# Performance work log

Hardware: AMD Instinct MI355X
Metric: run time of the kernel (lower is better)

## Reference

```python
import jax, jax.numpy as jnp
import numpy as np

NUM_HEADS = 8
HEAD_SIZE = 64  # hidden_dim // num_heads = 512 // 8
SCALE = 1.0 / np.sqrt(HEAD_SIZE).astype(np.float32)
CAUSAL = True


def setup_inputs() -> dict:
    key = jax.random.key(0)
    k1, k2, k3 = jax.random.split(key, 3)
    b, s, d = 4, 2048, 512
    x = jax.random.normal(k1, (b, s, d), dtype=jnp.float32)
    w_qkv = jax.random.normal(k2, (d, 3 * d), dtype=jnp.float32) * 0.02
    b_qkv = jnp.zeros((3 * d,), dtype=jnp.float32)
    w_out = jax.random.normal(k3, (d, d), dtype=jnp.float32) * 0.02
    b_out = jnp.zeros((d,), dtype=jnp.float32)
    return {"x": x, "w_qkv": w_qkv, "b_qkv": b_qkv, "w_out": w_out, "b_out": b_out}


def reference(x, w_qkv, b_qkv, w_out, b_out):
    b, s, d = x.shape
    h, hd = NUM_HEADS, HEAD_SIZE
    qkv = x @ w_qkv + b_qkv                      # (b, s, 3d)
    q, k, v = jnp.split(qkv, 3, axis=-1)
    # (b, s, d) -> (b, h, s, hd)
    q = q.reshape(b, s, h, hd).transpose(0, 2, 1, 3)
    k = k.reshape(b, s, h, hd).transpose(0, 2, 1, 3)
    v = v.reshape(b, s, h, hd).transpose(0, 2, 1, 3)
    scores = jnp.einsum('bhqd,bhkd->bhqk', q, k) * SCALE  # (b, h, s, s)
    if CAUSAL:
        causal_mask = jnp.triu(jnp.ones((s, s), dtype=bool), k=1)
        scores = jnp.where(causal_mask, -jnp.inf, scores)
    attn = jax.nn.softmax(scores, axis=-1)
    out = jnp.einsum('bhqk,bhkd->bhqd', attn, v)          # (b, h, s, hd)
    out = out.transpose(0, 2, 1, 3).reshape(b, s, d)
    return out @ w_out + b_out
```

## Files before the change

### kernel.cpp

```cpp
#include <hip/hip_runtime.h>
#include <hip/hip_bf16.h>

#define BATCH 4
#define SEQ   2048
#define DM    512
#define NH    8
#define HD    64
#define PART  (BATCH*NH*SEQ*HD)
#define QSCALE 0.18033688f

typedef unsigned short u16;
typedef unsigned int   u32;
typedef __bf16 bf16x8 __attribute__((ext_vector_type(8)));
typedef float  f32x4  __attribute__((ext_vector_type(4)));
typedef float  f32x16 __attribute__((ext_vector_type(16)));
typedef unsigned int u32x2 __attribute__((ext_vector_type(2)));

__device__ __forceinline__ u16 f2bf(float f) {
    union { float f; u32 u; } v; v.f = f;
    u32 r = v.u + 0x7fffu + ((v.u >> 16) & 1u);
    return (u16)(r >> 16);
}

__device__ __forceinline__ void glds16(const u16* g, u16* lds) {
    __builtin_amdgcn_global_load_lds(
        (const __attribute__((address_space(1))) void*)g,
        (__attribute__((address_space(3))) void*)lds, 16, 0, 0);
}

__device__ __forceinline__ void pl32swap(u32 &a, u32 &b) {
    u32x2 r = __builtin_amdgcn_permlane32_swap(a, b, false, false);
    a = r[0]; b = r[1];
}

__global__ __launch_bounds__(256) void prep_k(
    const float* __restrict__ x, u16* __restrict__ xb,
    const float* __restrict__ w_qkv, u16* __restrict__ t_qkv,
    const float* __restrict__ w_out, u16* __restrict__ t_out)
{
    __shared__ u16 Ts[64][72];
    const int z = blockIdx.z, bx = blockIdx.x, t = threadIdx.x;

    if (z == 0) {
        const int n8 = PART / 8;
        for (int i = bx * 256 + t; i < n8; i += 512 * 256) {
            float4 a = *(const float4*)(x + (size_t)i * 8);
            float4 b = *(const float4*)(x + (size_t)i * 8 + 4);
            union { uint4 v; u16 s[8]; } o;
            o.s[0] = f2bf(a.x); o.s[1] = f2bf(a.y);
            o.s[2] = f2bf(a.z); o.s[3] = f2bf(a.w);
            o.s[4] = f2bf(b.x); o.s[5] = f2bf(b.y);
            o.s[6] = f2bf(b.z); o.s[7] = f2bf(b.w);
            *(uint4*)(xb + (size_t)i * 8) = o.v;
        }
        return;
    }
    const int N = (z == 1) ? 3 * DM : DM;
    const int ntiles = N / 64;
    if (bx >= ntiles * 8) return;
    const float* W = (z == 1) ? w_qkv : w_out;
    u16* Wt = (z == 1) ? t_qkv : t_out;
    const int n0 = (bx % ntiles) * 64, k0 = (bx / ntiles) * 64;

    #pragma unroll
    for (int l = 0; l < 4; ++l) {
        int idx = l * 1024 + t * 4;
        int r = idx >> 6, c = idx & 63;
        float4 v = *(const float4*)(W + (size_t)(k0 + r) * N + n0 + c);
        Ts[c + 0][r] = f2bf(v.x);
        Ts[c + 1][r] = f2bf(v.y);
        Ts[c + 2][r] = f2bf(v.z);
        Ts[c + 3][r] = f2bf(v.w);
    }
    __syncthreads();
    #pragma unroll
    for (int l = 0; l < 2; ++l) {
        int idx = l * 256 + t;
        int row = idx >> 3, ch = idx & 7;
        *(uint4*)(Wt + (size_t)(n0 + row) * DM + k0 + ch * 8) =
            *(const uint4*)(&Ts[row][ch * 8]);
    }
}

template<int MODE>
__global__ __launch_bounds__(256) void gemm_k(
    const u16* __restrict__ A, const u16* __restrict__ Bt,
    const float* __restrict__ bias, void* __restrict__ outv,
    int M, int N, int K)
{
    constexpr int BM = (MODE == 1) ? 64 : 128;
    constexpr int NI = (MODE == 1) ? 2 : 4;

    __shared__ __align__(16) u16 As[2][BM * 32];
    __shared__ __align__(16) u16 Bs[2][128 * 32];

    const int tid  = threadIdx.x;
    const int bm0  = blockIdx.x * BM;
    const int bn0  = blockIdx.y * 128;
    const int wave = tid >> 6, lane = tid & 63;
    const int l16  = lane & 15, quad = lane >> 4;
    const int wr   = (MODE == 1) ? 0 : (wave & 1) * 64;
    const int wc   = (MODE == 1) ? wave * 32 : (wave >> 1) * 64;

    const int srow = (lane >> 2);
    const int scol = (lane & 3) * 8;
    const int arow = (MODE == 1) ? (wave * 16) : (wave * 32);
    const u16* Ag = A + (size_t)(bm0 + arow + srow) * K + scol;
    const u16* Bg = Bt + (size_t)(bn0 + wave * 32 + srow) * K + scol;
    const int wofsA = arow * 32;
    const int wofsB = (wave * 32) * 32;

    f32x4 acc[4][NI];
    #pragma unroll
    for (int i = 0; i < 4; ++i)
        #pragma unroll
        for (int j = 0; j < NI; ++j)
            acc[i][j] = (f32x4){0.f, 0.f, 0.f, 0.f};

    glds16(Ag, &As[0][wofsA]);
    if (MODE == 0) glds16(Ag + (size_t)16 * K, &As[0][wofsA + 16 * 32]);
    glds16(Bg,                  &Bs[0][wofsB]);
    glds16(Bg + (size_t)16 * K, &Bs[0][wofsB + 16 * 32]);
    __syncthreads();

    const int NIT = K >> 5;
    for (int it = 0; it < NIT; ++it) {
        const int cur = it & 1;
        if (it + 1 < NIT) {
            const int nx = cur ^ 1;
            const int k0 = (it + 1) << 5;
            glds16(Ag + k0, &As[nx][wofsA]);
            if (MODE == 0) glds16(Ag + k0 + (size_t)16 * K, &As[nx][wofsA + 16 * 32]);
            glds16(Bg + k0,                  &Bs[nx][wofsB]);
            glds16(Bg + k0 + (size_t)16 * K, &Bs[nx][wofsB + 16 * 32]);
        }

        bf16x8 af[4], bfr[NI];
        #pragma unroll
        for (int mi = 0; mi < 4; ++mi)
            af[mi] = *(const bf16x8*)(&As[cur][(wr + mi * 16 + l16) * 32 + quad * 8]);
        #pragma unroll
        for (int ni = 0; ni < NI; ++ni)
            bfr[ni] = *(const bf16x8*)(&Bs[cur][(wc + ni * 16 + l16) * 32 + quad * 8]);
        #pragma unroll
        for (int mi = 0; mi < 4; ++mi)
            #pragma unroll
            for (int ni = 0; ni < NI; ++ni)
                acc[mi][ni] = __builtin_amdgcn_mfma_f32_16x16x32_bf16(
                    af[mi], bfr[ni], acc[mi][ni], 0, 0, 0);
        __syncthreads();
    }

    #pragma unroll
    for (int mi = 0; mi < 4; ++mi) {
        #pragma unroll
        for (int ni = 0; ni < NI; ++ni) {
            int col = bn0 + wc + ni * 16 + l16;
            float bv = bias[col];
            int row0 = bm0 + wr + mi * 16 + quad * 4;
            float v[4];
            #pragma unroll
            for (int reg = 0; reg < 4; ++reg) v[reg] = acc[mi][ni][reg] + bv;

            if (MODE == 1) {
                #pragma unroll
                for (int reg = 0; reg < 4; ++reg)
                    ((float*)outv)[(size_t)(row0 + reg) * N + col] = v[reg];
            } else {
                u16* ws = (u16*)outv;
                int part = col >> 9, wi = col & 511;
                int h = wi >> 6, e = wi & 63;
                int b = row0 >> 11, s0 = row0 & 2047;
                if (part == 2) {
                    union { u16 q[4]; uint2 u; } pk;
                    #pragma unroll
                    for (int reg = 0; reg < 4; ++reg) pk.q[reg] = f2bf(v[reg]);
                    *(uint2*)(ws + (size_t)2 * PART +
                              ((size_t)(b * NH + h) * HD + e) * SEQ + s0) = pk.u;
                } else {
                    float scl = (part == 0) ? QSCALE : 1.0f;
                    #pragma unroll
                    for (int reg = 0; reg < 4; ++reg)
                        ws[(size_t)part * PART +
                           ((size_t)(b * NH + h) * SEQ + s0 + reg) * HD + e] =
                            f2bf(v[reg] * scl);
                }
            }
        }
    }
}

__global__ __launch_bounds__(256, 4) void attn_k(
    const u16* __restrict__ Q, const u16* __restrict__ K,
    const u16* __restrict__ Vt, u16* __restrict__ O)
{
    __shared__ __align__(16) u16 KsB[2][64 * 64];
    __shared__ __align__(16) u16 VtB[2][64 * 64];
    __shared__ float Lred[4][32];

    const int bh = blockIdx.x;
    const int qt = 31 - blockIdx.y;
    const int tid = threadIdx.x, wave = tid >> 6, lane = tid & 63;
    const int l31 = lane & 31, hi = lane >> 5, x7 = lane & 7;
    const int qh = wave >> 1, kh = wave & 1;
    const size_t baseK = (size_t)bh * SEQ * HD;
    const size_t baseV = (size_t)bh * HD * SEQ;
    const int b = bh >> 3, h = bh & 7;

    const int sub = lane >> 3;
    const int lcx = (lane & 7) ^ sub;
    const u16* kg = K  + baseK + (size_t)((wave * 16 + sub) * 64)   + lcx * 8;
    const u16* vg = Vt + baseV + (size_t)((wave * 16 + sub) * 2048) + lcx * 8;
    u16* ksd = &KsB[0][wave * 1024];
    u16* vtd = &VtB[0][wave * 1024];

    int koff[4], voff[2][2];
    #pragma unroll
    for (int k = 0; k < 4; ++k)
        koff[k] = (kh * 32 + l31) * 64 + ((((k << 1) + hi)) ^ x7) * 8;
    #pragma unroll
    for (int dt = 0; dt < 2; ++dt)
        #pragma unroll
        for (int k0 = 0; k0 < 2; ++k0)
            voff[dt][k0] = (dt * 32 + l31) * 64 + ((kh * 4 + k0 * 2 + hi) ^ x7) * 8;

    const u16* qg = Q + baseK + (size_t)(qt * 64 + qh * 32 + l31) * 64 + hi * 8;
    bf16x8 qf[4];
    #pragma unroll
    for (int k = 0; k < 4; ++k)
        qf[k] = *(const bf16x8*)(qg + k * 16);

    glds16(kg,            ksd);
    glds16(kg + 8 * 64,   ksd + 512);
    glds16(vg,            vtd);
    glds16(vg + 8 * 2048, vtd + 512);
    __syncthreads();

    float la0 = 0.f, la1 = 0.f;
    f32x16 o0, o1;
    #pragma unroll
    for (int i = 0; i < 16; ++i) { o0[i] = 0.f; o1[i] = 0.f; }

    for (int kt = 0; kt <= qt; ++kt) {
        const int cur = kt & 1;
        if (kt < qt) {
            const int nx = (cur ^ 1) * 4096;
            glds16(kg + (size_t)(kt + 1) * 4096,          ksd + nx);
            glds16(kg + (size_t)(kt + 1) * 4096 + 8 * 64, ksd + nx + 512);
            glds16(vg + (size_t)(kt + 1) * 64,            vtd + nx);
            glds16(vg + (size_t)(kt + 1) * 64 + 8 * 2048, vtd + nx + 512);
        }

        const bool diag = (kt == qt);
        if (!(diag && kh > qh)) {
            bf16x8 kf[4], vf[2][2];
            #pragma unroll
            for (int k = 0; k < 4; ++k)
                kf[k] = *(const bf16x8*)(&KsB[cur][koff[k]]);
            #pragma unroll
            for (int dt = 0; dt < 2; ++dt)
                #pragma unroll
                for (int k0 = 0; k0 < 2; ++k0)
                    vf[dt][k0] = *(const bf16x8*)(&VtB[cur][voff[dt][k0]]);

            f32x16 st;
            #pragma unroll
            for (int i = 0; i < 16; ++i) st[i] = 0.f;
            __builtin_amdgcn_s_setprio(1);
            #pragma unroll
            for (int k = 0; k < 4; ++k)
                st = __builtin_amdgcn_mfma_f32_32x32x16_bf16(
                    kf[k], qf[k], st, 0, 0, 0);
            __builtin_amdgcn_s_setprio(0);

            float p[16];
            #pragma unroll
            for (int r = 0; r < 16; ++r)
                p[r] = __builtin_amdgcn_exp2f(st[r]);
            if (diag && kh == qh) {
                #pragma unroll
                for (int r = 0; r < 16; ++r) {
                    int kvl = (r & 3) + 8 * (r >> 2) + 4 * hi;
                    if (kvl > l31) p[r] = 0.f;
                }
            }
            #pragma unroll
            for (int r = 0; r < 8; ++r) { la0 += p[r]; la1 += p[r + 8]; }

            u32 c[8];
            #pragma unroll
            for (int m = 0; m < 8; ++m) {
                __hip_bfloat162 t =
                    __float22bfloat162_rn(float2{p[2 * m], p[2 * m + 1]});
                c[m] = *(u32*)&t;
            }
            pl32swap(c[0], c[2]); pl32swap(c[1], c[3]);
            pl32swap(c[4], c[6]); pl32swap(c[5], c[7]);
            union { u32 w[4]; bf16x8 v; } pa0, pa1;
            pa0.w[0] = c[0]; pa0.w[1] = c[1]; pa0.w[2] = c[2]; pa0.w[3] = c[3];
            pa1.w[0] = c[4]; pa1.w[1] = c[5]; pa1.w[2] = c[6]; pa1.w[3] = c[7];

            __builtin_amdgcn_s_setprio(1);
            o0 = __builtin_amdgcn_mfma_f32_32x32x16_bf16(pa0.v, vf[0][0], o0, 0, 0, 0);
            o0 = __builtin_amdgcn_mfma_f32_32x32x16_bf16(pa1.v, vf[0][1], o0, 0, 0, 0);
            o1 = __builtin_amdgcn_mfma_f32_32x32x16_bf16(pa0.v, vf[1][0], o1, 0, 0, 0);
            o1 = __builtin_amdgcn_mfma_f32_32x32x16_bf16(pa1.v, vf[1][1], o1, 0, 0, 0);
            __builtin_amdgcn_s_setprio(0);
        }
        __syncthreads();
    }

    float l2 = (la0 + la1);
    l2 += __shfl_xor(l2, 32);
    if (lane < 32) Lred[wave][lane] = l2;
    float* Ob = (qh == 0) ? (float*)&KsB[0][0] : (float*)&VtB[0][0];
    if (kh == 1) {
        #pragma unroll
        for (int r = 0; r < 16; ++r) {
            Ob[r * 64 + lane]        = o0[r];
            Ob[(16 + r) * 64 + lane] = o1[r];
        }
    }
    __syncthreads();
    if (kh == 0) {
        #pragma unroll
        for (int r = 0; r < 16; ++r) {
            int ql = (r & 3) + 8 * (r >> 2) + 4 * hi;
            float lt = Lred[2 * qh][ql] + Lred[2 * qh + 1][ql];
            int srow = qt * 64 + qh * 32 + ql;
            size_t idx = (((size_t)(b * SEQ + srow)) * NH + h) * HD + l31;
            float v0 = (o0[r] + Ob[r * 64 + lane]) / lt;
            float v1 = (o1[r] + Ob[(16 + r) * 64 + lane]) / lt;
            O[idx]      = f2bf(v0);
            O[idx + 32] = f2bf(v1);
        }
    }
}

extern "C" void kernel_launch(void* const* d_in, const int* in_sizes, int n_in,
                              void* d_out, int out_size, void* d_ws, size_t ws_size,
                              hipStream_t stream) {
    const float* x     = (const float*)d_in[0];
    const float* w_qkv = (const float*)d_in[1];
    const float* b_qkv = (const float*)d_in[2];
    const float* w_out = (const float*)d_in[3];
    const float* b_out = (const float*)d_in[4];

    u16* qkv    = (u16*)d_ws;
    u16* attn   = qkv + (size_t)3 * PART;
    u16* xb     = attn + (size_t)PART;
    u16* wt_qkv = xb + (size_t)PART;
    u16* wt_out = wt_qkv + (size_t)(3 * DM) * DM;

    const int M = BATCH * SEQ;

    prep_k<<<dim3(512, 1, 3), 256, 0, stream>>>(x, xb, w_qkv, wt_qkv,
                                                w_out, wt_out);

    dim3 g1(M / 128, (3 * DM) / 128);
    gemm_k<0><<<g1, 256, 0, stream>>>(xb, wt_qkv, b_qkv, qkv, M, 3 * DM, DM);

    dim3 g2(BATCH * NH, 32);
    attn_k<<<g2, 256, 0, stream>>>(qkv, qkv + PART, qkv + 2 * (size_t)PART, attn);

    dim3 g3(M / 64, DM / 128);
    gemm_k<1><<<g3, 256, 0, stream>>>(attn, wt_out, b_out, (float*)d_out, M, DM, DM);
}
```

Before: 145.8 us.

## Fuse x fp32-to-bf16 conversion into QKV GEMM and stage V-transpose through LDS

Removes the separate x-to-bf16 conversion pass from the prep kernel. The QKV GEMM now loads fp32 x directly, converts it in registers and writes it to LDS, with the global loads issued before the MFMAs and the stores after them. Blocks that produce the V part now transpose their tile through LDS so the transposed V store uses coalesced 16-byte writes instead of scattered 8-byte writes. This saves one full read-plus-write pass over x, at the cost of twice the global read bytes for A inside the GEMM and extra VALU conversion work per iteration.

```diff
diff --git a/kernel.cpp b/kernel.cpp
--- a/kernel.cpp
+++ b/kernel.cpp
@@ -34,32 +34,16 @@
 }
 
 __global__ __launch_bounds__(256) void prep_k(
-    const float* __restrict__ x, u16* __restrict__ xb,
     const float* __restrict__ w_qkv, u16* __restrict__ t_qkv,
     const float* __restrict__ w_out, u16* __restrict__ t_out)
 {
     __shared__ u16 Ts[64][72];
     const int z = blockIdx.z, bx = blockIdx.x, t = threadIdx.x;
-
-    if (z == 0) {
-        const int n8 = PART / 8;
-        for (int i = bx * 256 + t; i < n8; i += 512 * 256) {
-            float4 a = *(const float4*)(x + (size_t)i * 8);
-            float4 b = *(const float4*)(x + (size_t)i * 8 + 4);
-            union { uint4 v; u16 s[8]; } o;
-            o.s[0] = f2bf(a.x); o.s[1] = f2bf(a.y);
-            o.s[2] = f2bf(a.z); o.s[3] = f2bf(a.w);
-            o.s[4] = f2bf(b.x); o.s[5] = f2bf(b.y);
-            o.s[6] = f2bf(b.z); o.s[7] = f2bf(b.w);
-            *(uint4*)(xb + (size_t)i * 8) = o.v;
-        }
-        return;
-    }
-    const int N = (z == 1) ? 3 * DM : DM;
+    const int N = (z == 0) ? 3 * DM : DM;
     const int ntiles = N / 64;
     if (bx >= ntiles * 8) return;
-    const float* W = (z == 1) ? w_qkv : w_out;
-    u16* Wt = (z == 1) ? t_qkv : t_out;
+    const float* W = (z == 0) ? w_qkv : w_out;
+    u16* Wt = (z == 0) ? t_qkv : t_out;
     const int n0 = (bx % ntiles) * 64, k0 = (bx / ntiles) * 64;
 
     #pragma unroll
@@ -84,15 +68,17 @@
 
 template<int MODE>
 __global__ __launch_bounds__(256) void gemm_k(
-    const u16* __restrict__ A, const u16* __restrict__ Bt,
+    const void* __restrict__ Araw, const u16* __restrict__ Bt,
     const float* __restrict__ bias, void* __restrict__ outv,
     int M, int N, int K)
 {
     constexpr int BM = (MODE == 1) ? 64 : 128;
     constexpr int NI = (MODE == 1) ? 2 : 4;
-
-    __shared__ __align__(16) u16 As[2][BM * 32];
-    __shared__ __align__(16) u16 Bs[2][128 * 32];
+    constexpr int ASZ = 2 * BM * 32;
+    constexpr int SMSZ = (MODE == 0) ? (128 * 136) : (ASZ + 2 * 128 * 32);
+    __shared__ __align__(16) u16 smem[SMSZ];
+    u16* AsB = smem;
+    u16* BsB = smem + ASZ;
 
     const int tid  = threadIdx.x;
     const int bm0  = blockIdx.x * BM;
@@ -105,10 +91,12 @@
     const int srow = (lane >> 2);
     const int scol = (lane & 3) * 8;
     const int arow = (MODE == 1) ? (wave * 16) : (wave * 32);
-    const u16* Ag = A + (size_t)(bm0 + arow + srow) * K + scol;
+    const float* Af = (const float*)Araw + (size_t)(bm0 + arow + srow) * K + scol;
+    const u16*   Ab = (const u16*)Araw + (size_t)(bm0 + arow + srow) * K + scol;
     const u16* Bg = Bt + (size_t)(bn0 + wave * 32 + srow) * K + scol;
     const int wofsA = arow * 32;
     const int wofsB = (wave * 32) * 32;
+    const int adst  = wofsA + lane * 8;
 
     f32x4 acc[4][NI];
     #pragma unroll
@@ -117,38 +105,102 @@
         for (int j = 0; j < NI; ++j)
             acc[i][j] = (f32x4){0.f, 0.f, 0.f, 0.f};
 
-    glds16(Ag, &As[0][wofsA]);
-    if (MODE == 0) glds16(Ag + (size_t)16 * K, &As[0][wofsA + 16 * 32]);
-    glds16(Bg,                  &Bs[0][wofsB]);
-    glds16(Bg + (size_t)16 * K, &Bs[0][wofsB + 16 * 32]);
+    if (MODE == 0) {
+        float4 a0 = *(const float4*)(Af);
+        float4 a1 = *(const float4*)(Af + 4);
+        float4 a2 = *(const float4*)(Af + 16 * K);
+        float4 a3 = *(const float4*)(Af + 16 * K + 4);
+        union { uint4 v; u16 s[8]; } o0, o1;
+        o0.s[0]=f2bf(a0.x); o0.s[1]=f2bf(a0.y); o0.s[2]=f2bf(a0.z); o0.s[3]=f2bf(a0.w);
+        o0.s[4]=f2bf(a1.x); o0.s[5]=f2bf(a1.y); o0.s[6]=f2bf(a1.z); o0.s[7]=f2bf(a1.w);
+        o1.s[0]=f2bf(a2.x); o1.s[1]=f2bf(a2.y); o1.s[2]=f2bf(a2.z); o1.s[3]=f2bf(a2.w);
+        o1.s[4]=f2bf(a3.x); o1.s[5]=f2bf(a3.y); o1.s[6]=f2bf(a3.z); o1.s[7]=f2bf(a3.w);
+        *(uint4*)(&AsB[adst])           = o0.v;
+        *(uint4*)(&AsB[adst + 16 * 32]) = o1.v;
+    } else {
+        glds16(Ab, &AsB[wofsA]);
+    }
+    glds16(Bg,                  &BsB[wofsB]);
+    glds16(Bg + (size_t)16 * K, &BsB[wofsB + 16 * 32]);
     __syncthreads();
 
     const int NIT = K >> 5;
     for (int it = 0; it < NIT; ++it) {
         const int cur = it & 1;
-        if (it + 1 < NIT) {
+        const bool pf = (it + 1 < NIT);
+        float4 a0, a1, a2, a3;
+        if (pf) {
             const int nx = cur ^ 1;
             const int k0 = (it + 1) << 5;
-            glds16(Ag + k0, &As[nx][wofsA]);
-            if (MODE == 0) glds16(Ag + k0 + (size_t)16 * K, &As[nx][wofsA + 16 * 32]);
-            glds16(Bg + k0,                  &Bs[nx][wofsB]);
-            glds16(Bg + k0 + (size_t)16 * K, &Bs[nx][wofsB + 16 * 32]);
+            glds16(Bg + k0,                  &BsB[nx * 4096 + wofsB]);
+            glds16(Bg + k0 + (size_t)16 * K, &BsB[nx * 4096 + wofsB + 16 * 32]);
+            if (MODE == 0) {
+                a0 = *(const float4*)(Af + k0);
+                a1 = *(const float4*)(Af + k0 + 4);
+                a2 = *(const float4*)(Af + k0 + 16 * K);
+                a3 = *(const float4*)(Af + k0 + 16 * K + 4);
+            } else {
+                glds16(Ab + k0, &AsB[nx * (BM * 32) + wofsA]);
+            }
         }
 
         bf16x8 af[4], bfr[NI];
         #pragma unroll
         for (int mi = 0; mi < 4; ++mi)
-            af[mi] = *(const bf16x8*)(&As[cur][(wr + mi * 16 + l16) * 32 + quad * 8]);
+            af[mi] = *(const bf16x8*)(&AsB[cur * (BM * 32) + (wr + mi * 16 + l16) * 32 + quad * 8]);
         #pragma unroll
         for (int ni = 0; ni < NI; ++ni)
-            bfr[ni] = *(const bf16x8*)(&Bs[cur][(wc + ni * 16 + l16) * 32 + quad * 8]);
+            bfr[ni] = *(const bf16x8*)(&BsB[cur * 4096 + (wc + ni * 16 + l16) * 32 + quad * 8]);
         #pragma unroll
         for (int mi = 0; mi < 4; ++mi)
             #pragma unroll
             for (int ni = 0; ni < NI; ++ni)
                 acc[mi][ni] = __builtin_amdgcn_mfma_f32_16x16x32_bf16(
                     af[mi], bfr[ni], acc[mi][ni], 0, 0, 0);
+
+        if (pf && MODE == 0) {
+            const int nx = cur ^ 1;
+            union { uint4 v; u16 s[8]; } o0, o1;
+            o0.s[0]=f2bf(a0.x); o0.s[1]=f2bf(a0.y); o0.s[2]=f2bf(a0.z); o0.s[3]=f2bf(a0.w);
+            o0.s[4]=f2bf(a1.x); o0.s[5]=f2bf(a1.y); o0.s[6]=f2bf(a1.z); o0.s[7]=f2bf(a1.w);
+            o1.s[0]=f2bf(a2.x); o1.s[1]=f2bf(a2.y); o1.s[2]=f2bf(a2.z); o1.s[3]=f2bf(a2.w);
+            o1.s[4]=f2bf(a3.x); o1.s[5]=f2bf(a3.y); o1.s[6]=f2bf(a3.z); o1.s[7]=f2bf(a3.w);
+            *(uint4*)(&AsB[nx * 4096 + adst])           = o0.v;
+            *(uint4*)(&AsB[nx * 4096 + adst + 16 * 32]) = o1.v;
+        }
         __syncthreads();
+    }
+
+    if (MODE == 0 && bn0 >= 1024) {
+        u16* T = smem;
+        #pragma unroll
+        for (int mi = 0; mi < 4; ++mi) {
+            #pragma unroll
+            for (int ni = 0; ni < NI; ++ni) {
+                int colL = wc + ni * 16 + l16;
+                float bv = bias[bn0 + colL];
+                int rowL = wr + mi * 16 + quad * 4;
+                union { u16 q[4]; uint2 u; } pk;
+                #pragma unroll
+                for (int reg = 0; reg < 4; ++reg)
+                    pk.q[reg] = f2bf(acc[mi][ni][reg] + bv);
+                *(uint2*)(&T[(size_t)colL * 136 + rowL]) = pk.u;
+            }
+        }
+        __syncthreads();
+        u16* ws2 = (u16*)outv + (size_t)2 * PART;
+        const int vn0 = bn0 - 1024;
+        const int b = bm0 >> 11;
+        const int s0v = bm0 & 2047;
+        const int colL = tid >> 1, half = tid & 1;
+        const int wi = vn0 + colL, h = wi >> 6, e = wi & 63;
+        u16* dst = ws2 + ((size_t)(b * NH + h) * HD + e) * SEQ + s0v + half * 64;
+        #pragma unroll
+        for (int j = 0; j < 8; ++j) {
+            *(uint4*)(dst + j * 8) =
+                *(const uint4*)(&T[(size_t)colL * 136 + half * 64 + j * 8]);
+        }
+        return;
     }
 
     #pragma unroll
@@ -171,20 +223,12 @@
                 int part = col >> 9, wi = col & 511;
                 int h = wi >> 6, e = wi & 63;
                 int b = row0 >> 11, s0 = row0 & 2047;
-                if (part == 2) {
-                    union { u16 q[4]; uint2 u; } pk;
-                    #pragma unroll
-                    for (int reg = 0; reg < 4; ++reg) pk.q[reg] = f2bf(v[reg]);
-                    *(uint2*)(ws + (size_t)2 * PART +
-                              ((size_t)(b * NH + h) * HD + e) * SEQ + s0) = pk.u;
-                } else {
-                    float scl = (part == 0) ? QSCALE : 1.0f;
-                    #pragma unroll
-                    for (int reg = 0; reg < 4; ++reg)
-                        ws[(size_t)part * PART +
-                           ((size_t)(b * NH + h) * SEQ + s0 + reg) * HD + e] =
-                            f2bf(v[reg] * scl);
-                }
+                float scl = (part == 0) ? QSCALE : 1.0f;
+                #pragma unroll
+                for (int reg = 0; reg < 4; ++reg)
+                    ws[(size_t)part * PART +
+                       ((size_t)(b * NH + h) * SEQ + s0 + reg) * HD + e] =
+                        f2bf(v[reg] * scl);
             }
         }
     }
@@ -348,17 +392,15 @@
 
     u16* qkv    = (u16*)d_ws;
     u16* attn   = qkv + (size_t)3 * PART;
-    u16* xb     = attn + (size_t)PART;
-    u16* wt_qkv = xb + (size_t)PART;
+    u16* wt_qkv = attn + (size_t)PART;
     u16* wt_out = wt_qkv + (size_t)(3 * DM) * DM;
 
     const int M = BATCH * SEQ;
 
-    prep_k<<<dim3(512, 1, 3), 256, 0, stream>>>(x, xb, w_qkv, wt_qkv,
-                                                w_out, wt_out);
+    prep_k<<<dim3(192, 1, 2), 256, 0, stream>>>(w_qkv, wt_qkv, w_out, wt_out);
 
     dim3 g1(M / 128, (3 * DM) / 128);
-    gemm_k<0><<<g1, 256, 0, stream>>>(xb, wt_qkv, b_qkv, qkv, M, 3 * DM, DM);
+    gemm_k<0><<<g1, 256, 0, stream>>>(x, wt_qkv, b_qkv, qkv, M, 3 * DM, DM);
 
     dim3 g2(BATCH * NH, 32);
     attn_k<<<g2, 256, 0, stream>>>(qkv, qkv + PART, qkv + 2 * (size_t)PART, attn);
```

After: 150.2 us. 1.03x slower.

## Split QKV GEMM into dedicated kernel with 256x256 tiles and swizzled LDS

Applied to the files above, without the earlier changes.

Replaces the templated GEMM for the QKV projection with a dedicated 512-thread kernel using 256x256 output tiles, 64-wide K steps, an XOR-swizzled LDS layout to avoid bank conflicts, and s_setprio around the MFMA bursts. The output GEMM becomes a plain specialized kernel. Larger tiles cut redundant global and LDS traffic, but the grid shrinks to 192 blocks, fewer than the CU count, and the 128 KB of LDS per block limits occupancy.

```diff
diff --git a/kernel.cpp b/kernel.cpp
--- a/kernel.cpp
+++ b/kernel.cpp
@@ -82,43 +82,150 @@
     }
 }
 
-template<int MODE>
-__global__ __launch_bounds__(256) void gemm_k(
+__global__ __launch_bounds__(512, 2) void gemm0_k(
     const u16* __restrict__ A, const u16* __restrict__ Bt,
-    const float* __restrict__ bias, void* __restrict__ outv,
+    const float* __restrict__ bias, u16* __restrict__ ws)
+{
+    __shared__ __align__(16) u16 As[2][256 * 64];
+    __shared__ __align__(16) u16 Bs[2][256 * 64];
+    const int K = 512;
+
+    const int tid = threadIdx.x, wave = tid >> 6, lane = tid & 63;
+    const int l16 = lane & 15, quad = (lane >> 4) & 3;
+    const int wm = wave >> 2, wn = wave & 3;
+    const int bm0 = blockIdx.x * 256, bn0 = blockIdx.y * 256;
+
+    const int srow8 = lane >> 3;
+    const int lcx   = (lane & 7) ^ srow8;
+    const u16* Agl = A  + (size_t)(bm0 + wave * 32 + srow8) * K + lcx * 8;
+    const u16* Bgl = Bt + (size_t)(bn0 + wave * 32 + srow8) * K + lcx * 8;
+    u16* adst = &As[0][wave * 2048];
+    u16* bdst = &Bs[0][wave * 2048];
+
+    int aoff[8][2], boff[4][2];
+    #pragma unroll
+    for (int mi = 0; mi < 8; ++mi)
+        #pragma unroll
+        for (int ks = 0; ks < 2; ++ks)
+            aoff[mi][ks] = (wm * 128 + mi * 16 + l16) * 64 +
+                           (((ks * 4 + quad)) ^ (l16 & 7)) * 8;
+    #pragma unroll
+    for (int ni = 0; ni < 4; ++ni)
+        #pragma unroll
+        for (int ks = 0; ks < 2; ++ks)
+            boff[ni][ks] = (wn * 64 + ni * 16 + l16) * 64 +
+                           (((ks * 4 + quad)) ^ (l16 & 7)) * 8;
+
+    f32x4 acc[8][4];
+    #pragma unroll
+    for (int i = 0; i < 8; ++i)
+        #pragma unroll
+        for (int j = 0; j < 4; ++j)
+            acc[i][j] = (f32x4){0.f, 0.f, 0.f, 0.f};
+
+    #pragma unroll
+    for (int i = 0; i < 4; ++i) {
+        glds16(Agl + (size_t)i * 8 * K, adst + i * 512);
+        glds16(Bgl + (size_t)i * 8 * K, bdst + i * 512);
+    }
+    __syncthreads();
+
+    for (int it = 0; it < 8; ++it) {
+        const int cur = it & 1;
+        if (it < 7) {
+            const int k0 = (it + 1) * 64;
+            const int nxo = (cur ^ 1) * 16384;
+            #pragma unroll
+            for (int i = 0; i < 4; ++i) {
+                glds16(Agl + k0 + (size_t)i * 8 * K, adst + nxo + i * 512);
+                glds16(Bgl + k0 + (size_t)i * 8 * K, bdst + nxo + i * 512);
+            }
+        }
+        const u16* Ab = &As[cur][0];
+        const u16* Bb = &Bs[cur][0];
+        #pragma unroll
+        for (int ks = 0; ks < 2; ++ks) {
+            bf16x8 bfr[4];
+            #pragma unroll
+            for (int ni = 0; ni < 4; ++ni)
+                bfr[ni] = *(const bf16x8*)(&Bb[boff[ni][ks]]);
+            __builtin_amdgcn_s_setprio(1);
+            #pragma unroll
+            for (int mi = 0; mi < 8; ++mi) {
+                bf16x8 af = *(const bf16x8*)(&Ab[aoff[mi][ks]]);
+                #pragma unroll
+                for (int ni = 0; ni < 4; ++ni)
+                    acc[mi][ni] = __builtin_amdgcn_mfma_f32_16x16x32_bf16(
+                        af, bfr[ni], acc[mi][ni], 0, 0, 0);
+            }
+            __builtin_amdgcn_s_setprio(0);
+        }
+        __syncthreads();
+    }
+
+    #pragma unroll
+    for (int mi = 0; mi < 8; ++mi) {
+        #pragma unroll
+        for (int ni = 0; ni < 4; ++ni) {
+            int col = bn0 + wn * 64 + ni * 16 + l16;
+            float bv = bias[col];
+            int row0 = bm0 + wm * 128 + mi * 16 + quad * 4;
+            float v[4];
+            #pragma unroll
+            for (int reg = 0; reg < 4; ++reg) v[reg] = acc[mi][ni][reg] + bv;
+
+            int part = col >> 9, wi = col & 511;
+            int h = wi >> 6, e = wi & 63;
+            int b = row0 >> 11, s0 = row0 & 2047;
+            if (part == 2) {
+                union { u16 q[4]; uint2 u; } pk;
+                #pragma unroll
+                for (int reg = 0; reg < 4; ++reg) pk.q[reg] = f2bf(v[reg]);
+                *(uint2*)(ws + (size_t)2 * PART +
+                          ((size_t)(b * NH + h) * HD + e) * SEQ + s0) = pk.u;
+            } else {
+                float scl = (part == 0) ? QSCALE : 1.0f;
+                #pragma unroll
+                for (int reg = 0; reg < 4; ++reg)
+                    ws[(size_t)part * PART +
+                       ((size_t)(b * NH + h) * SEQ + s0 + reg) * HD + e] =
+                        f2bf(v[reg] * scl);
+            }
+        }
+    }
+}
+
+__global__ __launch_bounds__(256) void gemm1_k(
+    const u16* __restrict__ A, const u16* __restrict__ Bt,
+    const float* __restrict__ bias, float* __restrict__ out,
     int M, int N, int K)
 {
-    constexpr int BM = (MODE == 1) ? 64 : 128;
-    constexpr int NI = (MODE == 1) ? 2 : 4;
-
-    __shared__ __align__(16) u16 As[2][BM * 32];
+    __shared__ __align__(16) u16 As[2][64 * 32];
     __shared__ __align__(16) u16 Bs[2][128 * 32];
 
     const int tid  = threadIdx.x;
-    const int bm0  = blockIdx.x * BM;
+    const int bm0  = blockIdx.x * 64;
     const int bn0  = blockIdx.y * 128;
     const int wave = tid >> 6, lane = tid & 63;
     const int l16  = lane & 15, quad = lane >> 4;
-    const int wr   = (MODE == 1) ? 0 : (wave & 1) * 64;
-    const int wc   = (MODE == 1) ? wave * 32 : (wave >> 1) * 64;
+    const int wc   = wave * 32;
 
     const int srow = (lane >> 2);
     const int scol = (lane & 3) * 8;
-    const int arow = (MODE == 1) ? (wave * 16) : (wave * 32);
+    const int arow = wave * 16;
     const u16* Ag = A + (size_t)(bm0 + arow + srow) * K + scol;
     const u16* Bg = Bt + (size_t)(bn0 + wave * 32 + srow) * K + scol;
     const int wofsA = arow * 32;
     const int wofsB = (wave * 32) * 32;
 
-    f32x4 acc[4][NI];
+    f32x4 acc[4][2];
     #pragma unroll
     for (int i = 0; i < 4; ++i)
         #pragma unroll
-        for (int j = 0; j < NI; ++j)
+        for (int j = 0; j < 2; ++j)
             acc[i][j] = (f32x4){0.f, 0.f, 0.f, 0.f};
 
     glds16(Ag, &As[0][wofsA]);
-    if (MODE == 0) glds16(Ag + (size_t)16 * K, &As[0][wofsA + 16 * 32]);
     glds16(Bg,                  &Bs[0][wofsB]);
     glds16(Bg + (size_t)16 * K, &Bs[0][wofsB + 16 * 32]);
     __syncthreads();
@@ -130,22 +237,21 @@
             const int nx = cur ^ 1;
             const int k0 = (it + 1) << 5;
             glds16(Ag + k0, &As[nx][wofsA]);
-            if (MODE == 0) glds16(Ag + k0 + (size_t)16 * K, &As[nx][wofsA + 16 * 32]);
             glds16(Bg + k0,                  &Bs[nx][wofsB]);
             glds16(Bg + k0 + (size_t)16 * K, &Bs[nx][wofsB + 16 * 32]);
         }
 
-        bf16x8 af[4], bfr[NI];
+        bf16x8 af[4], bfr[2];
         #pragma unroll
         for (int mi = 0; mi < 4; ++mi)
-            af[mi] = *(const bf16x8*)(&As[cur][(wr + mi * 16 + l16) * 32 + quad * 8]);
-        #pragma unroll
-        for (int ni = 0; ni < NI; ++ni)
+            af[mi] = *(const bf16x8*)(&As[cur][(mi * 16 + l16) * 32 + quad * 8]);
+        #pragma unroll
+        for (int ni = 0; ni < 2; ++ni)
             bfr[ni] = *(const bf16x8*)(&Bs[cur][(wc + ni * 16 + l16) * 32 + quad * 8]);
         #pragma unroll
         for (int mi = 0; mi < 4; ++mi)
             #pragma unroll
-            for (int ni = 0; ni < NI; ++ni)
+            for (int ni = 0; ni < 2; ++ni)
                 acc[mi][ni] = __builtin_amdgcn_mfma_f32_16x16x32_bf16(
                     af[mi], bfr[ni], acc[mi][ni], 0, 0, 0);
         __syncthreads();
@@ -154,38 +260,13 @@
     #pragma unroll
     for (int mi = 0; mi < 4; ++mi) {
         #pragma unroll
-        for (int ni = 0; ni < NI; ++ni) {
+        for (int ni = 0; ni < 2; ++ni) {
             int col = bn0 + wc + ni * 16 + l16;
             float bv = bias[col];
-            int row0 = bm0 + wr + mi * 16 + quad * 4;
-            float v[4];
-            #pragma unroll
-            for (int reg = 0; reg < 4; ++reg) v[reg] = acc[mi][ni][reg] + bv;
-
-            if (MODE == 1) {
-                #pragma unroll
-                for (int reg = 0; reg < 4; ++reg)
-                    ((float*)outv)[(size_t)(row0 + reg) * N + col] = v[reg];
-            } else {
-                u16* ws = (u16*)outv;
-                int part = col >> 9, wi = col & 511;
-                int h = wi >> 6, e = wi & 63;
-                int b = row0 >> 11, s0 = row0 & 2047;
-                if (part == 2) {
-                    union { u16 q[4]; uint2 u; } pk;
-                    #pragma unroll
-                    for (int reg = 0; reg < 4; ++reg) pk.q[reg] = f2bf(v[reg]);
-                    *(uint2*)(ws + (size_t)2 * PART +
-                              ((size_t)(b * NH + h) * HD + e) * SEQ + s0) = pk.u;
-                } else {
-                    float scl = (part == 0) ? QSCALE : 1.0f;
-                    #pragma unroll
-                    for (int reg = 0; reg < 4; ++reg)
-                        ws[(size_t)part * PART +
-                           ((size_t)(b * NH + h) * SEQ + s0 + reg) * HD + e] =
-                            f2bf(v[reg] * scl);
-                }
-            }
+            int row0 = bm0 + mi * 16 + quad * 4;
+            #pragma unroll
+            for (int reg = 0; reg < 4; ++reg)
+                out[(size_t)(row0 + reg) * N + col] = acc[mi][ni][reg] + bv;
         }
     }
 }
@@ -357,12 +438,12 @@
     prep_k<<<dim3(512, 1, 3), 256, 0, stream>>>(x, xb, w_qkv, wt_qkv,
                                                 w_out, wt_out);
 
-    dim3 g1(M / 128, (3 * DM) / 128);
-    gemm_k<0><<<g1, 256, 0, stream>>>(xb, wt_qkv, b_qkv, qkv, M, 3 * DM, DM);
+    dim3 g1(M / 256, (3 * DM) / 256);
+    gemm0_k<<<g1, 512, 0, stream>>>(xb, wt_qkv, b_qkv, qkv);
 
     dim3 g2(BATCH * NH, 32);
     attn_k<<<g2, 256, 0, stream>>>(qkv, qkv + PART, qkv + 2 * (size_t)PART, attn);
 
     dim3 g3(M / 64, DM / 128);
-    gemm_k<1><<<g3, 256, 0, stream>>>(attn, wt_out, b_out, (float*)d_out, M, DM, DM);
-}
+    gemm1_k<<<g3, 256, 0, stream>>>(attn, wt_out, b_out, (float*)d_out, M, DM, DM);
+}
```

Result: slower. 151.1 us (+3.6%).
